# Kernel optimization log

Measured on AMD Instinct MI355X. Metric: run time of the kernel, lower is better.

## Reference

```python
import jax, jax.numpy as jnp
import numpy as np

U1 = 512
U2 = 512
BATCH = 8192
INPUT_DIM = (U1 + U2) * 3  # 3072
UNITS = U2 * 3             # 1536


def _build_mask():
    """Replicates the block-structured random 0/1 unit_diags construction.

    Unit blocks (rows): [0,U2), [U2,2U2), [2U2,3U2).
    Input blocks (cols): ds1,ds2,ds3 of width U1 each, then stn1,stn2,stn3 of width U2.
    Each (unit-block, input-block) pair has a fixed Bernoulli keep-probability
    derived from the original randint(2)/randint(4) logic.
    """
    rng = np.random.default_rng(0)
    col_edges = [0, U1, 2 * U1, 3 * U1, 3 * U1 + U2, 3 * U1 + 2 * U2, 3 * U1 + 3 * U2]
    # keep-probabilities per unit-block (rows) x input-block (cols)
    probs = [
        [1.0, 0.5, 0.0, 1.0, 0.5, 0.0],   # units [0, U2)
        [0.5, 0.75, 0.5, 0.5, 0.75, 0.5], # units [U2, 2U2): randint(4)>0 -> p=0.75
        [0.0, 0.5, 1.0, 0.0, 0.5, 1.0],   # units [2U2, 3U2)
    ]
    p = np.zeros((UNITS, INPUT_DIM), dtype=np.float32)
    for ub in range(3):
        for j in range(6):
            p[ub * U2:(ub + 1) * U2, col_edges[j]:col_edges[j + 1]] = probs[ub][j]
    mask = (rng.random((UNITS, INPUT_DIM)) < p).astype(np.float32)
    return mask


def setup_inputs() -> dict:
    key = jax.random.key(0)
    k1, k2 = jax.random.split(key)
    x = jax.random.normal(k1, (BATCH, INPUT_DIM), dtype=jnp.float32)
    # w_init = uniform(0, 0.01), non-negative constrained
    w = jax.random.uniform(k2, (INPUT_DIM, UNITS), dtype=jnp.float32, minval=0.0, maxval=0.01)
    # gpi_bias = [0, 0] -> bias initialized to zeros
    b = jnp.zeros((UNITS,), dtype=jnp.float32)
    mask = jnp.asarray(_build_mask())  # (UNITS, INPUT_DIM), fixed 0/1 constants
    return {"x": x, "w": w, "b": b, "mask": mask}


def reference(x, w, b, mask):
    # Original: p[b,u,:] = mask[u,:] * x[b,:] ;  f = diag_part(p @ w) + b
    # => f[b,u] = sum_i mask[u,i] * x[b,i] * w[i,u] + b[u]
    # Collapses to a masked linear: x @ (mask.T * w) + b
    return x @ (mask.T * w) + b
```

## Files before the change

kernel.cpp:

```cpp
#include <hip/hip_runtime.h>
#include <stdint.h>

#define MDIM 8192
#define NDIM 1536
#define KDIM 3072

#define BM 256
#define BN 128
#define BK 64
#define NGB ((MDIM / BM) * (NDIM / BN))

#define NMB ((KDIM / 64) * (NDIM / 64))
#define NCVT ((MDIM * KDIM / 4) / 256)

typedef unsigned short u16;
typedef float  f32x4  __attribute__((ext_vector_type(4)));
typedef __bf16 bf16x8 __attribute__((ext_vector_type(8)));

__device__ __forceinline__ u16 f2bf(float f) {
    union { float f; unsigned int u; } v; v.f = f;
    unsigned int u = v.u;
    return (u16)((u + 0x7fffu + ((u >> 16) & 1u)) >> 16);
}

__global__ void prep_kernel(const float* __restrict__ w, const float* __restrict__ mask,
                            u16* __restrict__ Bt,
                            const float4* __restrict__ x, ushort4* __restrict__ xb) {
    const int t = threadIdx.x;
    if (blockIdx.x < NMB) {
        __shared__ float sw[64][65];
        const int kb = blockIdx.x % (KDIM / 64);
        const int nb = blockIdx.x / (KDIM / 64);
        const int k0 = kb * 64, n0 = nb * 64;
        {
            const int c4 = t & 15;
            const int r  = t >> 4;
#pragma unroll
            for (int rr = 0; rr < 4; ++rr) {
                int row = rr * 16 + r;
                float4 v = *(const float4*)&w[(size_t)(k0 + row) * NDIM + n0 + c4 * 4];
                sw[row][c4 * 4 + 0] = v.x;
                sw[row][c4 * 4 + 1] = v.y;
                sw[row][c4 * 4 + 2] = v.z;
                sw[row][c4 * 4 + 3] = v.w;
            }
        }
        __syncthreads();
        {
            const int n  = t >> 2;
            const int ks = (t & 3) * 16;
#pragma unroll
            for (int j = 0; j < 4; ++j) {
                int k = ks + j * 4;
                float4 mv = *(const float4*)&mask[(size_t)(n0 + n) * KDIM + k0 + k];
                ushort4 o;
                o.x = f2bf(mv.x * sw[k + 0][n]);
                o.y = f2bf(mv.y * sw[k + 1][n]);
                o.z = f2bf(mv.z * sw[k + 2][n]);
                o.w = f2bf(mv.w * sw[k + 3][n]);
                *(ushort4*)&Bt[(size_t)(n0 + n) * KDIM + k0 + k] = o;
            }
        }
    } else {
        int i = (blockIdx.x - NMB) * 256 + t;
        float4 v = x[i];
        ushort4 o;
        o.x = f2bf(v.x); o.y = f2bf(v.y); o.z = f2bf(v.z); o.w = f2bf(v.w);
        xb[i] = o;
    }
}

__device__ __forceinline__ void gload_lds16(const void* g, void* l) {
    __builtin_amdgcn_global_load_lds(
        (const __attribute__((address_space(1))) unsigned int*)g,
        (__attribute__((address_space(3))) unsigned int*)l, 16, 0, 0);
}

#define BARR  __builtin_amdgcn_s_barrier()
#define PRIO1 __builtin_amdgcn_s_setprio(1)
#define PRIO0 __builtin_amdgcn_s_setprio(0)
#define VM(n) asm volatile("s_waitcnt vmcnt(" #n ")" ::: "memory")

__global__ void __launch_bounds__(512, 2)
gemm_kernel(const u16* __restrict__ Ag,
            const u16* __restrict__ Bg,
            const float* __restrict__ bias,
            float* __restrict__ C) {
    extern __shared__ u16 smem[];
    u16* sAb = smem;
    u16* sBb = smem + 32768;

    const int tid  = threadIdx.x;
    const int wv   = tid >> 6;
    const int lane = tid & 63;

    const int bik = blockIdx.x;
    int bx, by;
    if (bik < 128) {
        by = (bik & 7) * 4 + ((bik >> 3) & 3);
        bx = 4 + (bik >> 5);
    } else {
        const int s = bik - 128;
        by = (s & 7) * 4 + ((s >> 3) & 3);
        const int r = s >> 5;
        bx = r < 4 ? r : r + 4;
    }
    const int m0 = by * BM, n0 = bx * BN;
    const int cls = bx >> 2;

    int ksplit, kb0, kb1, NT;
    if (cls == 1)      { ksplit = 48; kb0 = 0;   kb1 = 0;    NT = 48; }
    else if (cls == 0) { ksplit = 16; kb0 = 0;   kb1 = 1536; NT = 32; }
    else               { ksplit = 16; kb0 = 512; kb1 = 2048; NT = 32; }
    const int NI = NT >> 1;
    auto kof = [&](int i) { return i < ksplit ? kb0 + i * 64 : kb1 + (i - ksplit) * 64; };

    const int srow = lane >> 2;
    const int scol = ((lane & 3) ^ ((lane >> 3) & 3)) * 8;
    const u16* gA = Ag + (size_t)(m0 + wv * 16 + srow) * KDIM + scol;
    const u16* gB = Bg + (size_t)(n0 + wv * 16 + srow) * KDIM + scol;
    u16* dA0 = &sAb[(wv * 16) * 32];
    u16* dA1 = &sAb[(wv * 16 + 128) * 32];
    u16* dB  = &sBb[(wv * 16) * 32];

#define SA(b, p, ki) { gload_lds16(gA + (ki) + (p) * 32,                     dA0 + ((b) * 2 + (p)) * 8192); \
                       gload_lds16(gA + (ki) + (p) * 32 + (size_t)128 * KDIM, dA1 + ((b) * 2 + (p)) * 8192); }
#define SB(b, p, ki)   gload_lds16(gB + (ki) + (p) * 32,                     dB  + ((b) * 2 + (p)) * 4096);

    const int wm = (wv >> 1) * 64;
    const int wn = (wv & 1) * 64;
    const int fr = lane & 15;
    const int fq = lane >> 4;
    const int fsw = (fq ^ ((fr >> 1) & 3)) * 8;

#define AFRAG(b, kk, mt) (*(const bf16x8*)&sAb[(((b) * 2 + (kk)) * 256 + wm + (mt) * 16 + fr) * 32 + fsw])
#define BFRAG(b, kk, nt) (*(const bf16x8*)&sBb[(((b) * 2 + (kk)) * 128 + wn + (nt) * 16 + fr) * 32 + fsw])
#define MF(mt, nt, xa, xb_) acc[mt][nt] = __builtin_amdgcn_mfma_f32_16x16x32_bf16(xa, xb_, acc[mt][nt], 0, 0, 0)
#define M8(mA, mB, xA, xB, b0_, b1_, b2_, b3_) \
    MF(mA, 0, xA, b0_); MF(mA, 1, xA, b1_); MF(mA, 2, xA, b2_); MF(mA, 3, xA, b3_); \
    MF(mB, 0, xB, b0_); MF(mB, 1, xB, b1_); MF(mB, 2, xB, b2_); MF(mB, 3, xB, b3_);

    f32x4 acc[4][4] = {};

    {
        const int k0 = kof(0), k1 = kof(1);
        SB(0, 0, k0); SA(0, 0, k0); SB(0, 1, k0); SA(0, 1, k0);
        SB(1, 0, k1); SA(1, 0, k1); SB(1, 1, k1);
    }
    VM(4);
    BARR;

#define QUAD(bb, S1, S2, S3, S4, VW)                                              \
    {                                                                             \
        { S1; }                                                                   \
        {                                                                         \
            bf16x8 b0 = BFRAG(bb, 0, 0), b1 = BFRAG(bb, 0, 1),                    \
                   b2 = BFRAG(bb, 0, 2), b3 = BFRAG(bb, 0, 3);                    \
            bf16x8 a0 = AFRAG(bb, 0, 0), a1 = AFRAG(bb, 0, 1);                    \
            BARR; PRIO1; M8(0, 1, a0, a1, b0, b1, b2, b3); PRIO0; BARR;           \
            { S2; }                                                               \
            bf16x8 a2 = AFRAG(bb, 0, 2), a3 = AFRAG(bb, 0, 3);                    \
            BARR; PRIO1; M8(2, 3, a2, a3, b0, b1, b2, b3); PRIO0; BARR;           \
        }                                                                         \
        { S3; }                                                                   \
        {                                                                         \
            bf16x8 b0 = BFRAG(bb, 1, 0), b1 = BFRAG(bb, 1, 1),                    \
                   b2 = BFRAG(bb, 1, 2), b3 = BFRAG(bb, 1, 3);                    \
            bf16x8 a0 = AFRAG(bb, 1, 0), a1 = AFRAG(bb, 1, 1);                    \
            BARR; PRIO1; M8(0, 1, a0, a1, b0, b1, b2, b3); PRIO0; BARR;           \
            { S4; }                                                               \
            bf16x8 a2 = AFRAG(bb, 1, 2), a3 = AFRAG(bb, 1, 3);                    \
            BARR; PRIO1; M8(2, 3, a2, a3, b0, b1, b2, b3); PRIO0;                 \
            { VW; }                                                               \
            BARR;                                                                 \
        }                                                                         \
    }

    for (int i = 0; i < NI; ++i) {
        const bool nl  = (i + 1 < NI);
        const int  kn1 = kof(2 * i + 1);
        const int  kn2 = nl ? kof(2 * i + 2) : 0;
        const int  kn3 = nl ? kof(2 * i + 3) : 0;

        QUAD(0,
             SA(1, 1, kn1),
             if (nl) { SB(0, 0, kn2); },
             if (nl) { SA(0, 0, kn2); },
             if (nl) { SB(0, 1, kn2); },
             if (nl) { VM(4); } else { VM(0); });

        QUAD(1,
             if (nl) { SA(0, 1, kn2); },
             if (nl) { SB(1, 0, kn3); },
             if (nl) { SA(1, 0, kn3); },
             if (nl) { SB(1, 1, kn3); },
             if (nl) { VM(4); });
    }

#pragma unroll
    for (int nt = 0; nt < 4; ++nt) {
        int n = n0 + wn + nt * 16 + fr;
        float bv = bias[n];
#pragma unroll
        for (int mt = 0; mt < 4; ++mt) {
            int m = m0 + wm + mt * 16 + fq * 4;
#pragma unroll
            for (int r = 0; r < 4; ++r)
                C[(size_t)(m + r) * NDIM + n] = acc[mt][nt][r] + bv;
        }
    }
}

extern "C" void kernel_launch(void* const* d_in, const int* in_sizes, int n_in,
                              void* d_out, int out_size, void* d_ws, size_t ws_size,
                              hipStream_t stream) {
    const float* x    = (const float*)d_in[0];
    const float* w    = (const float*)d_in[1];
    const float* bias = (const float*)d_in[2];
    const float* mask = (const float*)d_in[3];
    float* out = (float*)d_out;

    u16* xb = (u16*)d_ws;
    u16* Bt = (u16*)((char*)d_ws + (size_t)50331648);

    static bool attr_done = false;
    if (!attr_done) {
        (void)hipFuncSetAttribute((const void*)gemm_kernel,
                                  hipFuncAttributeMaxDynamicSharedMemorySize, 98304);
        attr_done = true;
    }

    prep_kernel<<<NMB + NCVT, 256, 0, stream>>>(w, mask, Bt, (const float4*)x, (ushort4*)xb);
    gemm_kernel<<<NGB, 512, 98304, stream>>>(xb, Bt, bias, out);
}
```

Measured before the change: 255.7 us.

## Split-K the dense middle column blocks across two workgroups with flag handoff

The middle unit block needs the full K range (48 tiles) while the other blocks use 32, which leaves the tail imbalanced. This change splits each middle-block tile into two workgroups of 24 K-tiles each, raising the grid from 384 to 512 workgroups. The first half writes C plus bias and sets a flag. The second half spins on that flag and then adds its partial sum with a read-modify-write. The flags are stored inside the Bt workspace, at offsets chosen to land on zero-mask regions that are assumed to stay zero. This relies on that zero assumption and on both halves being co-resident, and it adds an extra C read and write pass.

```diff
diff --git a/kernel.cpp b/kernel.cpp
--- a/kernel.cpp
+++ b/kernel.cpp
@@ -8,7 +8,7 @@
 #define BM 256
 #define BN 128
 #define BK 64
-#define NGB ((MDIM / BM) * (NDIM / BN))
+#define NGB 512
 
 #define NMB ((KDIM / 64) * (NDIM / 64))
 #define NCVT ((MDIM * KDIM / 4) / 256)
@@ -83,9 +83,10 @@
 
 __global__ void __launch_bounds__(512, 2)
 gemm_kernel(const u16* __restrict__ Ag,
-            const u16* __restrict__ Bg,
+            const u16* Bg,
             const float* __restrict__ bias,
-            float* __restrict__ C) {
+            float* __restrict__ C,
+            unsigned* flags) {
     extern __shared__ u16 smem[];
     u16* sAb = smem;
     u16* sBb = smem + 32768;
@@ -95,21 +96,24 @@
     const int lane = tid & 63;
 
     const int bik = blockIdx.x;
-    int bx, by;
-    if (bik < 128) {
-        by = (bik & 7) * 4 + ((bik >> 3) & 3);
-        bx = 4 + (bik >> 5);
+    int bx, by, cls, half = 0, fullidx = 0;
+    if (bik < 256) {
+        fullidx = bik & 127;
+        half    = bik >> 7;
+        by = (fullidx & 7) * 4 + ((fullidx >> 3) & 3);
+        bx = 4 + (fullidx >> 5);
+        cls = 1;
     } else {
-        const int s = bik - 128;
+        const int s = bik - 256;
         by = (s & 7) * 4 + ((s >> 3) & 3);
         const int r = s >> 5;
         bx = r < 4 ? r : r + 4;
+        cls = bx >> 2;
     }
     const int m0 = by * BM, n0 = bx * BN;
-    const int cls = bx >> 2;
 
     int ksplit, kb0, kb1, NT;
-    if (cls == 1)      { ksplit = 48; kb0 = 0;   kb1 = 0;    NT = 48; }
+    if (cls == 1)      { ksplit = 24; kb0 = half ? 1536 : 0; kb1 = 0; NT = 24; }
     else if (cls == 0) { ksplit = 16; kb0 = 0;   kb1 = 1536; NT = 32; }
     else               { ksplit = 16; kb0 = 512; kb1 = 2048; NT = 32; }
     const int NI = NT >> 1;
@@ -197,16 +201,54 @@
              if (nl) { VM(4); });
     }
 
-#pragma unroll
-    for (int nt = 0; nt < 4; ++nt) {
-        int n = n0 + wn + nt * 16 + fr;
-        float bv = bias[n];
-#pragma unroll
-        for (int mt = 0; mt < 4; ++mt) {
-            int m = m0 + wm + mt * 16 + fq * 4;
-#pragma unroll
-            for (int r = 0; r < 4; ++r)
-                C[(size_t)(m + r) * NDIM + n] = acc[mt][nt][r] + bv;
+    if (cls != 1) {
+#pragma unroll
+        for (int nt = 0; nt < 4; ++nt) {
+            int n = n0 + wn + nt * 16 + fr;
+            float bv = bias[n];
+#pragma unroll
+            for (int mt = 0; mt < 4; ++mt) {
+                int m = m0 + wm + mt * 16 + fq * 4;
+#pragma unroll
+                for (int r = 0; r < 4; ++r)
+                    C[(size_t)(m + r) * NDIM + n] = acc[mt][nt][r] + bv;
+            }
+        }
+    } else {
+        unsigned* flag = flags + (size_t)fullidx * 1536 + 512;
+        if (half == 0) {
+#pragma unroll
+            for (int nt = 0; nt < 4; ++nt) {
+                int n = n0 + wn + nt * 16 + fr;
+                float bv = bias[n];
+#pragma unroll
+                for (int mt = 0; mt < 4; ++mt) {
+                    int m = m0 + wm + mt * 16 + fq * 4;
+#pragma unroll
+                    for (int r = 0; r < 4; ++r)
+                        C[(size_t)(m + r) * NDIM + n] = acc[mt][nt][r] + bv;
+                }
+            }
+            __threadfence();
+            __syncthreads();
+            if (tid == 0) atomicExch(flag, 1u);
+        } else {
+            if (tid == 0) { while (atomicAdd(flag, 0u) == 0u) __builtin_amdgcn_s_sleep(8); }
+            __syncthreads();
+            __threadfence();
+#pragma unroll
+            for (int nt = 0; nt < 4; ++nt) {
+                int n = n0 + wn + nt * 16 + fr;
+#pragma unroll
+                for (int mt = 0; mt < 4; ++mt) {
+                    int m = m0 + wm + mt * 16 + fq * 4;
+#pragma unroll
+                    for (int r = 0; r < 4; ++r) {
+                        size_t idx = (size_t)(m + r) * NDIM + n;
+                        C[idx] = C[idx] + acc[mt][nt][r];
+                    }
+                }
+            }
         }
     }
 }
@@ -231,5 +273,5 @@
     }
 
     prep_kernel<<<NMB + NCVT, 256, 0, stream>>>(w, mask, Bt, (const float4*)x, (ushort4*)xb);
-    gemm_kernel<<<NGB, 512, 98304, stream>>>(xb, Bt, bias, out);
-}
+    gemm_kernel<<<NGB, 512, 98304, stream>>>(xb, Bt, bias, out, (unsigned*)Bt);
+}
```

Measured after the change: 320.3 us. +25.3%, slower.

## Halve GEMM M-tile to 128 and raise occupancy to four blocks per CU

Applied to the files above, without the earlier changes.

Shrinks the block tile from 256x128 to 128x128, so each wave holds a 2x4 accumulator grid instead of 4x4. Shared memory drops to 64KB and launch bounds now allow four blocks per CU. The block-index remap, load macros, fragment indexing and vmcnt waits are reworked to match. The goal is more resident blocks and a finer-grained grid to balance the uneven K-work classes, at the cost of less data reuse per tile and more global traffic for B.

```diff
diff --git a/kernel.cpp b/kernel.cpp
--- a/kernel.cpp
+++ b/kernel.cpp
@@ -5,7 +5,7 @@
 #define NDIM 1536
 #define KDIM 3072
 
-#define BM 256
+#define BM 128
 #define BN 128
 #define BK 64
 #define NGB ((MDIM / BM) * (NDIM / BN))
@@ -81,32 +81,35 @@
 #define PRIO0 __builtin_amdgcn_s_setprio(0)
 #define VM(n) asm volatile("s_waitcnt vmcnt(" #n ")" ::: "memory")
 
-__global__ void __launch_bounds__(512, 2)
+#define PLANE 4096
+
+__global__ void __launch_bounds__(512, 4)
 gemm_kernel(const u16* __restrict__ Ag,
             const u16* __restrict__ Bg,
             const float* __restrict__ bias,
             float* __restrict__ C) {
     extern __shared__ u16 smem[];
     u16* sAb = smem;
-    u16* sBb = smem + 32768;
+    u16* sBb = smem + 16384;
 
     const int tid  = threadIdx.x;
     const int wv   = tid >> 6;
     const int lane = tid & 63;
 
     const int bik = blockIdx.x;
-    int bx, by;
-    if (bik < 128) {
-        by = (bik & 7) * 4 + ((bik >> 3) & 3);
-        bx = 4 + (bik >> 5);
+    int bx, by, cls;
+    if (bik < 256) {
+        by = (bik & 7) * 8 + ((bik >> 3) & 7);
+        bx = 4 + (bik >> 6);
+        cls = 1;
     } else {
-        const int s = bik - 128;
-        by = (s & 7) * 4 + ((s >> 3) & 3);
-        const int r = s >> 5;
-        bx = r < 4 ? r : r + 4;
+        const int s = bik - 256;
+        by = (s & 7) * 8 + ((s >> 3) & 7);
+        const int b = s >> 6;
+        bx = b < 4 ? b : b + 4;
+        cls = bx >> 2;
     }
     const int m0 = by * BM, n0 = bx * BN;
-    const int cls = bx >> 2;
 
     int ksplit, kb0, kb1, NT;
     if (cls == 1)      { ksplit = 48; kb0 = 0;   kb1 = 0;    NT = 48; }
@@ -119,61 +122,53 @@
     const int scol = ((lane & 3) ^ ((lane >> 3) & 3)) * 8;
     const u16* gA = Ag + (size_t)(m0 + wv * 16 + srow) * KDIM + scol;
     const u16* gB = Bg + (size_t)(n0 + wv * 16 + srow) * KDIM + scol;
-    u16* dA0 = &sAb[(wv * 16) * 32];
-    u16* dA1 = &sAb[(wv * 16 + 128) * 32];
-    u16* dB  = &sBb[(wv * 16) * 32];
-
-#define SA(b, p, ki) { gload_lds16(gA + (ki) + (p) * 32,                     dA0 + ((b) * 2 + (p)) * 8192); \
-                       gload_lds16(gA + (ki) + (p) * 32 + (size_t)128 * KDIM, dA1 + ((b) * 2 + (p)) * 8192); }
-#define SB(b, p, ki)   gload_lds16(gB + (ki) + (p) * 32,                     dB  + ((b) * 2 + (p)) * 4096);
-
-    const int wm = (wv >> 1) * 64;
+    u16* dA = &sAb[(wv * 16) * 32];
+    u16* dB = &sBb[(wv * 16) * 32];
+
+#define SA(b, p, ki) gload_lds16(gA + (ki) + (p) * 32, dA + ((b) * 2 + (p)) * PLANE);
+#define SB(b, p, ki) gload_lds16(gB + (ki) + (p) * 32, dB + ((b) * 2 + (p)) * PLANE);
+
+    const int wm = (wv >> 1) * 32;
     const int wn = (wv & 1) * 64;
     const int fr = lane & 15;
     const int fq = lane >> 4;
     const int fsw = (fq ^ ((fr >> 1) & 3)) * 8;
 
-#define AFRAG(b, kk, mt) (*(const bf16x8*)&sAb[(((b) * 2 + (kk)) * 256 + wm + (mt) * 16 + fr) * 32 + fsw])
+#define AFRAG(b, kk, mt) (*(const bf16x8*)&sAb[(((b) * 2 + (kk)) * 128 + wm + (mt) * 16 + fr) * 32 + fsw])
 #define BFRAG(b, kk, nt) (*(const bf16x8*)&sBb[(((b) * 2 + (kk)) * 128 + wn + (nt) * 16 + fr) * 32 + fsw])
 #define MF(mt, nt, xa, xb_) acc[mt][nt] = __builtin_amdgcn_mfma_f32_16x16x32_bf16(xa, xb_, acc[mt][nt], 0, 0, 0)
-#define M8(mA, mB, xA, xB, b0_, b1_, b2_, b3_) \
-    MF(mA, 0, xA, b0_); MF(mA, 1, xA, b1_); MF(mA, 2, xA, b2_); MF(mA, 3, xA, b3_); \
-    MF(mB, 0, xB, b0_); MF(mB, 1, xB, b1_); MF(mB, 2, xB, b2_); MF(mB, 3, xB, b3_);
-
-    f32x4 acc[4][4] = {};
+#define M4(xa0, xa1, xb0, xb1, ntA, ntB) \
+    MF(0, ntA, xa0, xb0); MF(0, ntB, xa0, xb1); \
+    MF(1, ntA, xa1, xb0); MF(1, ntB, xa1, xb1);
+
+    f32x4 acc[2][4] = {};
 
     {
         const int k0 = kof(0), k1 = kof(1);
         SB(0, 0, k0); SA(0, 0, k0); SB(0, 1, k0); SA(0, 1, k0);
         SB(1, 0, k1); SA(1, 0, k1); SB(1, 1, k1);
     }
-    VM(4);
+    VM(3);
     BARR;
 
 #define QUAD(bb, S1, S2, S3, S4, VW)                                              \
     {                                                                             \
         { S1; }                                                                   \
-        {                                                                         \
-            bf16x8 b0 = BFRAG(bb, 0, 0), b1 = BFRAG(bb, 0, 1),                    \
-                   b2 = BFRAG(bb, 0, 2), b3 = BFRAG(bb, 0, 3);                    \
-            bf16x8 a0 = AFRAG(bb, 0, 0), a1 = AFRAG(bb, 0, 1);                    \
-            BARR; PRIO1; M8(0, 1, a0, a1, b0, b1, b2, b3); PRIO0; BARR;           \
-            { S2; }                                                               \
-            bf16x8 a2 = AFRAG(bb, 0, 2), a3 = AFRAG(bb, 0, 3);                    \
-            BARR; PRIO1; M8(2, 3, a2, a3, b0, b1, b2, b3); PRIO0; BARR;           \
-        }                                                                         \
+        bf16x8 a0 = AFRAG(bb, 0, 0), a1 = AFRAG(bb, 0, 1);                        \
+        bf16x8 b0 = BFRAG(bb, 0, 0), b1 = BFRAG(bb, 0, 1),                        \
+               b2 = BFRAG(bb, 0, 2), b3 = BFRAG(bb, 0, 3);                        \
+        BARR; PRIO1; M4(a0, a1, b0, b1, 0, 1); PRIO0; BARR;                       \
+        { S2; }                                                                   \
+        BARR; PRIO1; M4(a0, a1, b2, b3, 2, 3); PRIO0; BARR;                       \
         { S3; }                                                                   \
-        {                                                                         \
-            bf16x8 b0 = BFRAG(bb, 1, 0), b1 = BFRAG(bb, 1, 1),                    \
-                   b2 = BFRAG(bb, 1, 2), b3 = BFRAG(bb, 1, 3);                    \
-            bf16x8 a0 = AFRAG(bb, 1, 0), a1 = AFRAG(bb, 1, 1);                    \
-            BARR; PRIO1; M8(0, 1, a0, a1, b0, b1, b2, b3); PRIO0; BARR;           \
-            { S4; }                                                               \
-            bf16x8 a2 = AFRAG(bb, 1, 2), a3 = AFRAG(bb, 1, 3);                    \
-            BARR; PRIO1; M8(2, 3, a2, a3, b0, b1, b2, b3); PRIO0;                 \
-            { VW; }                                                               \
-            BARR;                                                                 \
-        }                                                                         \
+        bf16x8 c0 = AFRAG(bb, 1, 0), c1 = AFRAG(bb, 1, 1);                        \
+        bf16x8 d0 = BFRAG(bb, 1, 0), d1 = BFRAG(bb, 1, 1),                        \
+               d2 = BFRAG(bb, 1, 2), d3 = BFRAG(bb, 1, 3);                        \
+        BARR; PRIO1; M4(c0, c1, d0, d1, 0, 1); PRIO0; BARR;                       \
+        { S4; }                                                                   \
+        BARR; PRIO1; M4(c0, c1, d2, d3, 2, 3); PRIO0;                             \
+        { VW; }                                                                   \
+        BARR;                                                                     \
     }
 
     for (int i = 0; i < NI; ++i) {
@@ -187,14 +182,14 @@
              if (nl) { SB(0, 0, kn2); },
              if (nl) { SA(0, 0, kn2); },
              if (nl) { SB(0, 1, kn2); },
-             if (nl) { VM(4); } else { VM(0); });
+             if (nl) { VM(3); } else { VM(0); });
 
         QUAD(1,
              if (nl) { SA(0, 1, kn2); },
              if (nl) { SB(1, 0, kn3); },
              if (nl) { SA(1, 0, kn3); },
              if (nl) { SB(1, 1, kn3); },
-             if (nl) { VM(4); });
+             if (nl) { VM(3); });
     }
 
 #pragma unroll
@@ -202,7 +197,7 @@
         int n = n0 + wn + nt * 16 + fr;
         float bv = bias[n];
 #pragma unroll
-        for (int mt = 0; mt < 4; ++mt) {
+        for (int mt = 0; mt < 2; ++mt) {
             int m = m0 + wm + mt * 16 + fq * 4;
 #pragma unroll
             for (int r = 0; r < 4; ++r)
@@ -226,10 +221,10 @@
     static bool attr_done = false;
     if (!attr_done) {
         (void)hipFuncSetAttribute((const void*)gemm_kernel,
-                                  hipFuncAttributeMaxDynamicSharedMemorySize, 98304);
+                                  hipFuncAttributeMaxDynamicSharedMemorySize, 65536);
         attr_done = true;
     }
 
     prep_kernel<<<NMB + NCVT, 256, 0, stream>>>(w, mask, Bt, (const float4*)x, (ushort4*)xb);
-    gemm_kernel<<<NGB, 512, 98304, stream>>>(xb, Bt, bias, out);
-}
+    gemm_kernel<<<NGB, 512, 65536, stream>>>(xb, Bt, bias, out);
+}
```

Result: no change. 258.6 us (+1.2%).

## Split dense middle column tiles into narrower 256x64 tiles to balance work

Applied to the files above, without the earlier changes.

The middle unit block (cls 1) needs the full K range (48 k-steps), while the outer blocks skip zero mask regions (32 k-steps). This creates load imbalance across workgroups. The change adds a separate gemm_full path that uses 256x64 tiles for the middle columns, so those are covered by 256 narrower blocks, and raises the grid from 384 to 512 workgroups. It aims to even out per-block runtime and fill the CUs better, at the cost of lower B reuse and more A traffic for the middle region.

```diff
diff --git a/kernel.cpp b/kernel.cpp
--- a/kernel.cpp
+++ b/kernel.cpp
@@ -4,11 +4,6 @@
 #define MDIM 8192
 #define NDIM 1536
 #define KDIM 3072
-
-#define BM 256
-#define BN 128
-#define BK 64
-#define NGB ((MDIM / BM) * (NDIM / BN))
 
 #define NMB ((KDIM / 64) * (NDIM / 64))
 #define NCVT ((MDIM * KDIM / 4) / 256)
@@ -81,40 +76,12 @@
 #define PRIO0 __builtin_amdgcn_s_setprio(0)
 #define VM(n) asm volatile("s_waitcnt vmcnt(" #n ")" ::: "memory")
 
-__global__ void __launch_bounds__(512, 2)
-gemm_kernel(const u16* __restrict__ Ag,
-            const u16* __restrict__ Bg,
-            const float* __restrict__ bias,
-            float* __restrict__ C) {
-    extern __shared__ u16 smem[];
+__device__ __forceinline__ void gemm_skip(const u16* __restrict__ Ag, const u16* __restrict__ Bg,
+                                          const float* __restrict__ bias, float* __restrict__ C,
+                                          u16* smem, int m0, int n0, int kb0, int kb1, int tid) {
     u16* sAb = smem;
     u16* sBb = smem + 32768;
-
-    const int tid  = threadIdx.x;
-    const int wv   = tid >> 6;
-    const int lane = tid & 63;
-
-    const int bik = blockIdx.x;
-    int bx, by;
-    if (bik < 128) {
-        by = (bik & 7) * 4 + ((bik >> 3) & 3);
-        bx = 4 + (bik >> 5);
-    } else {
-        const int s = bik - 128;
-        by = (s & 7) * 4 + ((s >> 3) & 3);
-        const int r = s >> 5;
-        bx = r < 4 ? r : r + 4;
-    }
-    const int m0 = by * BM, n0 = bx * BN;
-    const int cls = bx >> 2;
-
-    int ksplit, kb0, kb1, NT;
-    if (cls == 1)      { ksplit = 48; kb0 = 0;   kb1 = 0;    NT = 48; }
-    else if (cls == 0) { ksplit = 16; kb0 = 0;   kb1 = 1536; NT = 32; }
-    else               { ksplit = 16; kb0 = 512; kb1 = 2048; NT = 32; }
-    const int NI = NT >> 1;
-    auto kof = [&](int i) { return i < ksplit ? kb0 + i * 64 : kb1 + (i - ksplit) * 64; };
-
+    const int wv = tid >> 6, lane = tid & 63;
     const int srow = lane >> 2;
     const int scol = ((lane & 3) ^ ((lane >> 3) & 3)) * 8;
     const u16* gA = Ag + (size_t)(m0 + wv * 16 + srow) * KDIM + scol;
@@ -123,9 +90,9 @@
     u16* dA1 = &sAb[(wv * 16 + 128) * 32];
     u16* dB  = &sBb[(wv * 16) * 32];
 
-#define SA(b, p, ki) { gload_lds16(gA + (ki) + (p) * 32,                     dA0 + ((b) * 2 + (p)) * 8192); \
-                       gload_lds16(gA + (ki) + (p) * 32 + (size_t)128 * KDIM, dA1 + ((b) * 2 + (p)) * 8192); }
-#define SB(b, p, ki)   gload_lds16(gB + (ki) + (p) * 32,                     dB  + ((b) * 2 + (p)) * 4096);
+#define SSA(b, p, ki) { gload_lds16(gA + (ki) + (p) * 32,                      dA0 + ((b) * 2 + (p)) * 8192); \
+                        gload_lds16(gA + (ki) + (p) * 32 + (size_t)128 * KDIM, dA1 + ((b) * 2 + (p)) * 8192); }
+#define SSB(b, p, ki)   gload_lds16(gB + (ki) + (p) * 32,                      dB  + ((b) * 2 + (p)) * 4096);
 
     const int wm = (wv >> 1) * 64;
     const int wn = (wv & 1) * 64;
@@ -133,68 +100,67 @@
     const int fq = lane >> 4;
     const int fsw = (fq ^ ((fr >> 1) & 3)) * 8;
 
-#define AFRAG(b, kk, mt) (*(const bf16x8*)&sAb[(((b) * 2 + (kk)) * 256 + wm + (mt) * 16 + fr) * 32 + fsw])
-#define BFRAG(b, kk, nt) (*(const bf16x8*)&sBb[(((b) * 2 + (kk)) * 128 + wn + (nt) * 16 + fr) * 32 + fsw])
-#define MF(mt, nt, xa, xb_) acc[mt][nt] = __builtin_amdgcn_mfma_f32_16x16x32_bf16(xa, xb_, acc[mt][nt], 0, 0, 0)
-#define M8(mA, mB, xA, xB, b0_, b1_, b2_, b3_) \
-    MF(mA, 0, xA, b0_); MF(mA, 1, xA, b1_); MF(mA, 2, xA, b2_); MF(mA, 3, xA, b3_); \
-    MF(mB, 0, xB, b0_); MF(mB, 1, xB, b1_); MF(mB, 2, xB, b2_); MF(mB, 3, xB, b3_);
+#define SAF(b, kk, mt) (*(const bf16x8*)&sAb[(((b) * 2 + (kk)) * 256 + wm + (mt) * 16 + fr) * 32 + fsw])
+#define SBF(b, kk, nt) (*(const bf16x8*)&sBb[(((b) * 2 + (kk)) * 128 + wn + (nt) * 16 + fr) * 32 + fsw])
+#define SMF(mt, nt, xa, xb_) acc[mt][nt] = __builtin_amdgcn_mfma_f32_16x16x32_bf16(xa, xb_, acc[mt][nt], 0, 0, 0)
+#define SM8(mA, mB, xA, xB, b0_, b1_, b2_, b3_) \
+    SMF(mA, 0, xA, b0_); SMF(mA, 1, xA, b1_); SMF(mA, 2, xA, b2_); SMF(mA, 3, xA, b3_); \
+    SMF(mB, 0, xB, b0_); SMF(mB, 1, xB, b1_); SMF(mB, 2, xB, b2_); SMF(mB, 3, xB, b3_);
 
     f32x4 acc[4][4] = {};
+    auto kof = [&](int i) { return i < 16 ? kb0 + i * 64 : kb1 + (i - 16) * 64; };
 
     {
         const int k0 = kof(0), k1 = kof(1);
-        SB(0, 0, k0); SA(0, 0, k0); SB(0, 1, k0); SA(0, 1, k0);
-        SB(1, 0, k1); SA(1, 0, k1); SB(1, 1, k1);
+        SSB(0, 0, k0); SSA(0, 0, k0); SSB(0, 1, k0); SSA(0, 1, k0);
+        SSB(1, 0, k1); SSA(1, 0, k1); SSB(1, 1, k1);
     }
     VM(4);
     BARR;
 
-#define QUAD(bb, S1, S2, S3, S4, VW)                                              \
+#define SKQUAD(bb, S1, S2, S3, S4, VW)                                            \
     {                                                                             \
         { S1; }                                                                   \
         {                                                                         \
-            bf16x8 b0 = BFRAG(bb, 0, 0), b1 = BFRAG(bb, 0, 1),                    \
-                   b2 = BFRAG(bb, 0, 2), b3 = BFRAG(bb, 0, 3);                    \
-            bf16x8 a0 = AFRAG(bb, 0, 0), a1 = AFRAG(bb, 0, 1);                    \
-            BARR; PRIO1; M8(0, 1, a0, a1, b0, b1, b2, b3); PRIO0; BARR;           \
+            bf16x8 b0 = SBF(bb, 0, 0), b1 = SBF(bb, 0, 1),                        \
+                   b2 = SBF(bb, 0, 2), b3 = SBF(bb, 0, 3);                        \
+            bf16x8 a0 = SAF(bb, 0, 0), a1 = SAF(bb, 0, 1);                        \
+            BARR; PRIO1; SM8(0, 1, a0, a1, b0, b1, b2, b3); PRIO0; BARR;          \
             { S2; }                                                               \
-            bf16x8 a2 = AFRAG(bb, 0, 2), a3 = AFRAG(bb, 0, 3);                    \
-            BARR; PRIO1; M8(2, 3, a2, a3, b0, b1, b2, b3); PRIO0; BARR;           \
+            bf16x8 a2 = SAF(bb, 0, 2), a3 = SAF(bb, 0, 3);                        \
+            BARR; PRIO1; SM8(2, 3, a2, a3, b0, b1, b2, b3); PRIO0; BARR;          \
         }                                                                         \
         { S3; }                                                                   \
         {                                                                         \
-            bf16x8 b0 = BFRAG(bb, 1, 0), b1 = BFRAG(bb, 1, 1),                    \
-                   b2 = BFRAG(bb, 1, 2), b3 = BFRAG(bb, 1, 3);                    \
-            bf16x8 a0 = AFRAG(bb, 1, 0), a1 = AFRAG(bb, 1, 1);                    \
-            BARR; PRIO1; M8(0, 1, a0, a1, b0, b1, b2, b3); PRIO0; BARR;           \
+            bf16x8 b0 = SBF(bb, 1, 0), b1 = SBF(bb, 1, 1),                        \
+                   b2 = SBF(bb, 1, 2), b3 = SBF(bb, 1, 3);                        \
+            bf16x8 a0 = SAF(bb, 1, 0), a1 = SAF(bb, 1, 1);                        \
+            BARR; PRIO1; SM8(0, 1, a0, a1, b0, b1, b2, b3); PRIO0; BARR;          \
             { S4; }                                                               \
-            bf16x8 a2 = AFRAG(bb, 1, 2), a3 = AFRAG(bb, 1, 3);                    \
-            BARR; PRIO1; M8(2, 3, a2, a3, b0, b1, b2, b3); PRIO0;                 \
+            bf16x8 a2 = SAF(bb, 1, 2), a3 = SAF(bb, 1, 3);                        \
+            BARR; PRIO1; SM8(2, 3, a2, a3, b0, b1, b2, b3); PRIO0;                \
             { VW; }                                                               \
             BARR;                                                                 \
         }                                                                         \
     }
 
-    for (int i = 0; i < NI; ++i) {
-        const bool nl  = (i + 1 < NI);
+    for (int i = 0; i < 16; ++i) {
+        const bool nl  = (i + 1 < 16);
         const int  kn1 = kof(2 * i + 1);
         const int  kn2 = nl ? kof(2 * i + 2) : 0;
         const int  kn3 = nl ? kof(2 * i + 3) : 0;
-
-        QUAD(0,
-             SA(1, 1, kn1),
-             if (nl) { SB(0, 0, kn2); },
-             if (nl) { SA(0, 0, kn2); },
-             if (nl) { SB(0, 1, kn2); },
-             if (nl) { VM(4); } else { VM(0); });
-
-        QUAD(1,
-             if (nl) { SA(0, 1, kn2); },
-             if (nl) { SB(1, 0, kn3); },
-             if (nl) { SA(1, 0, kn3); },
-             if (nl) { SB(1, 1, kn3); },
-             if (nl) { VM(4); });
+        SKQUAD(0,
+               SSA(1, 1, kn1),
+               if (nl) { SSB(0, 0, kn2); },
+               if (nl) { SSA(0, 0, kn2); },
+               if (nl) { SSB(0, 1, kn2); },
+               if (nl) { VM(4); } else { VM(0); });
+        SKQUAD(1,
+               if (nl) { SSA(0, 1, kn2); },
+               if (nl) { SSB(1, 0, kn3); },
+               if (nl) { SSA(1, 0, kn3); },
+               if (nl) { SSB(1, 1, kn3); },
+               if (nl) { VM(4); });
     }
 
 #pragma unroll
@@ -208,6 +174,115 @@
             for (int r = 0; r < 4; ++r)
                 C[(size_t)(m + r) * NDIM + n] = acc[mt][nt][r] + bv;
         }
+    }
+}
+
+__device__ __forceinline__ void gemm_full(const u16* __restrict__ Ag, const u16* __restrict__ Bg,
+                                          const float* __restrict__ bias, float* __restrict__ C,
+                                          u16* smem, int m0, int n0, int tid) {
+    u16* sAb = smem;
+    u16* sB6 = smem + 32768;
+    const int wv = tid >> 6, lane = tid & 63;
+    const int srow = lane >> 2;
+    const int scol = ((lane & 3) ^ ((lane >> 3) & 3)) * 8;
+    const u16* gA = Ag + (size_t)(m0 + wv * 16 + srow) * KDIM + scol;
+    const u16* gB = Bg + (size_t)(n0 + (wv & 3) * 16 + srow) * KDIM + scol;
+    u16* dA0 = &sAb[(wv * 16) * 32];
+    u16* dA1 = &sAb[(wv * 16 + 128) * 32];
+    u16* dB6 = &sB6[((wv & 3) * 16) * 32];
+    const int bp = wv >> 2;
+
+#define FSA(b, p, ki) { gload_lds16(gA + (ki) + (p) * 32,                      dA0 + ((b) * 2 + (p)) * 8192); \
+                        gload_lds16(gA + (ki) + (p) * 32 + (size_t)128 * KDIM, dA1 + ((b) * 2 + (p)) * 8192); }
+#define FSB(b, ki)      gload_lds16(gB + (ki) + bp * 32,                       dB6 + ((b) * 2 + bp) * 2048);
+
+    const int wm = (wv >> 1) * 64;
+    const int wn = (wv & 1) * 32;
+    const int fr = lane & 15;
+    const int fq = lane >> 4;
+    const int fsw = (fq ^ ((fr >> 1) & 3)) * 8;
+
+#define FAF(b, kk, mt) (*(const bf16x8*)&sAb[(((b) * 2 + (kk)) * 256 + wm + (mt) * 16 + fr) * 32 + fsw])
+#define FBF(b, kk, nt) (*(const bf16x8*)&sB6[(((b) * 2 + (kk)) * 64  + wn + (nt) * 16 + fr) * 32 + fsw])
+#define FMF(mt, nt, xa, xb_) acc[mt][nt] = __builtin_amdgcn_mfma_f32_16x16x32_bf16(xa, xb_, acc[mt][nt], 0, 0, 0)
+#define FM8(a0_, a1_, a2_, a3_, b0_, b1_) \
+    FMF(0, 0, a0_, b0_); FMF(0, 1, a0_, b1_); FMF(1, 0, a1_, b0_); FMF(1, 1, a1_, b1_); \
+    FMF(2, 0, a2_, b0_); FMF(2, 1, a2_, b1_); FMF(3, 0, a3_, b0_); FMF(3, 1, a3_, b1_);
+
+    f32x4 acc[4][2] = {};
+
+    FSB(0, 0); FSA(0, 0, 0); FSA(0, 1, 0); FSA(1, 0, 64);
+    VM(2);
+    BARR;
+
+#define FQUAD(bb, T1, T2, VW)                                                     \
+    {                                                                             \
+        { T1; }                                                                   \
+        {                                                                         \
+            bf16x8 a0 = FAF(bb, 0, 0), a1 = FAF(bb, 0, 1),                        \
+                   a2 = FAF(bb, 0, 2), a3 = FAF(bb, 0, 3);                        \
+            bf16x8 b0 = FBF(bb, 0, 0), b1 = FBF(bb, 0, 1);                        \
+            BARR; PRIO1; FM8(a0, a1, a2, a3, b0, b1); PRIO0; BARR;                \
+        }                                                                         \
+        { T2; }                                                                   \
+        {                                                                         \
+            bf16x8 a0 = FAF(bb, 1, 0), a1 = FAF(bb, 1, 1),                        \
+                   a2 = FAF(bb, 1, 2), a3 = FAF(bb, 1, 3);                        \
+            bf16x8 b0 = FBF(bb, 1, 0), b1 = FBF(bb, 1, 1);                        \
+            BARR; PRIO1; FM8(a0, a1, a2, a3, b0, b1); PRIO0;                      \
+            { VW; }                                                               \
+            BARR;                                                                 \
+        }                                                                         \
+    }
+
+    for (int i = 0; i < 24; ++i) {
+        const bool nl = (i + 1 < 24);
+        const int k1 = (2 * i + 1) * 64;
+        const int k2 = nl ? (2 * i + 2) * 64 : 0;
+        const int k3 = nl ? (2 * i + 3) * 64 : 0;
+        FQUAD(0,
+              { FSA(1, 1, k1); FSB(1, k1); },
+              { if (nl) { FSA(0, 0, k2); } },
+              { if (nl) { VM(2); } else { VM(0); } });
+        FQUAD(1,
+              { if (nl) { FSB(0, k2); FSA(0, 1, k2); } },
+              { if (nl) { FSA(1, 0, k3); } },
+              { if (nl) { VM(2); } else { VM(0); } });
+    }
+
+#pragma unroll
+    for (int nt = 0; nt < 2; ++nt) {
+        int n = n0 + wn + nt * 16 + fr;
+        float bv = bias[n];
+#pragma unroll
+        for (int mt = 0; mt < 4; ++mt) {
+            int m = m0 + wm + mt * 16 + fq * 4;
+#pragma unroll
+            for (int r = 0; r < 4; ++r)
+                C[(size_t)(m + r) * NDIM + n] = acc[mt][nt][r] + bv;
+        }
+    }
+}
+
+__global__ void __launch_bounds__(512, 2)
+gemm_kernel(const u16* __restrict__ Ag, const u16* __restrict__ Bg,
+            const float* __restrict__ bias, float* __restrict__ C) {
+    extern __shared__ u16 smem[];
+    const int tid = threadIdx.x;
+    const int bik = blockIdx.x;
+    if (bik >= 128 && bik < 384) {
+        const int s    = bik - 128;
+        const int half = s >> 7;
+        const int t_   = s & 127;
+        const int by   = (t_ & 7) * 4 + ((t_ >> 3) & 3);
+        const int bx   = (half ? 8 : 0) + (t_ >> 5);
+        gemm_skip(Ag, Bg, bias, C, smem, by * 256, bx * 128,
+                  half ? 512 : 0, half ? 2048 : 1536, tid);
+    } else {
+        const int f   = bik < 128 ? bik : bik - 256;
+        const int by  = (f & 7) * 4 + ((f >> 3) & 3);
+        const int col = f >> 5;
+        gemm_full(Ag, Bg, bias, C, smem, by * 256, 512 + col * 64, tid);
     }
 }
 
@@ -231,5 +306,5 @@
     }
 
     prep_kernel<<<NMB + NCVT, 256, 0, stream>>>(w, mask, Bt, (const float4*)x, (ushort4*)xb);
-    gemm_kernel<<<NGB, 512, 98304, stream>>>(xb, Bt, bias, out);
-}
+    gemm_kernel<<<512, 512, 98304, stream>>>(xb, Bt, bias, out);
+}
```

New measurement: 263.6 us. +3.1%, slower.
